# Kernel optimization log

Hardware: AMD Instinct MI355X
Metric: run time of the kernel (lower is better)

Reference implementation:

```python
import jax, jax.numpy as jnp
import numpy as np

B, S = 4096, 128
POS_RANK, DIR_RANK = 10, 4
WIDTH = 256
POS_DIM = POS_RANK * 6  # 60
DIR_DIM = DIR_RANK * 6  # 24
SKIPS = (4,)


def _pe(x, rank):
    # x: [N, 3] -> [N, 6*rank]; sin/cos of x scaled by 2^i for i in 0..rank-1
    freqs = (2.0 ** jnp.arange(rank)).astype(x.dtype)        # [L]
    xf = x[..., None] * freqs                                 # [N, 3, L]
    enc = jnp.concatenate([jnp.sin(xf), jnp.cos(xf)], axis=-1)  # [N, 3, 2L]
    return enc.reshape(x.shape[0], -1)


def _linear_init(key, fan_in, fan_out):
    k1, k2 = jax.random.split(key)
    bound = 1.0 / np.sqrt(fan_in)
    W = jax.random.uniform(k1, (fan_in, fan_out), jnp.float32, -bound, bound)
    b = jax.random.uniform(k2, (fan_out,), jnp.float32, -bound, bound)
    return W, b


def setup_inputs() -> dict:
    key = jax.random.key(0)
    ks = jax.random.split(key, 16)
    inp = {
        "input_pos": jax.random.normal(ks[0], (B, S, 3), jnp.float32),
        "input_dir": jax.random.normal(ks[1], (B, S, 3), jnp.float32),
    }
    # trunk layers: in-dims follow skip-concat structure
    in_dims = [POS_DIM] + [WIDTH + POS_DIM if (i in SKIPS) else WIDTH for i in range(7)]
    for i, d_in in enumerate(in_dims):
        W, b = _linear_init(ks[2 + i], d_in, WIDTH)
        inp[f"W{i}"] = W
        inp[f"b{i}"] = b
    inp["Wd"], inp["bd"] = _linear_init(ks[10], WIDTH, 1)
    inp["Wc0"], inp["bc0"] = _linear_init(ks[11], WIDTH + DIR_DIM, WIDTH // 2)
    inp["Wc1"], inp["bc1"] = _linear_init(ks[12], WIDTH // 2, 3)
    return inp


def reference(input_pos, input_dir,
              W0, b0, W1, b1, W2, b2, W3, b3, W4, b4, W5, b5, W6, b6, W7, b7,
              Wd, bd, Wc0, bc0, Wc1, bc1):
    Ws = [W0, W1, W2, W3, W4, W5, W6, W7]
    bs = [b0, b1, b2, b3, b4, b5, b6, b7]
    b, s, _ = input_pos.shape
    embed_pos = _pe(input_pos.reshape(-1, 3), POS_RANK)  # [N, 60]
    embed_dir = _pe(input_dir.reshape(-1, 3), DIR_RANK)  # [N, 24]
    hx = embed_pos
    for i, (W, bb) in enumerate(zip(Ws, bs)):
        hx = jax.nn.relu(hx @ W + bb)
        if i in SKIPS:
            hx = jnp.concatenate([hx, embed_pos], axis=1)
    density = (hx @ Wd + bd).reshape(b, s)
    dir_feat = jnp.concatenate([hx, embed_dir], axis=1)  # [N, 280]
    color = (jax.nn.relu(dir_feat @ Wc0 + bc0) @ Wc1 + bc1).reshape(b, s, 3)
    return density, color
```

## Files before the change

kernel.cpp:

```cpp
#include <hip/hip_runtime.h>
#include <hip/hip_bf16.h>

using bf16 = __bf16;
typedef __bf16 bf16x8 __attribute__((ext_vector_type(8)));
typedef __bf16 bf16x4 __attribute__((ext_vector_type(4)));
typedef float  f32x4  __attribute__((ext_vector_type(4)));

#define MFMA16(a, b, c) __builtin_amdgcn_mfma_f32_16x16x32_bf16((a), (b), (c), 0, 0, 0)

constexpr int P0  = 0;
constexpr int P1  = 16384;
constexpr int P2  = 81920;
constexpr int P3  = 147456;
constexpr int P4  = 212992;
constexpr int P5  = 278528;
constexpr int P6  = 360448;
constexpr int P7  = 425984;
constexpr int PD  = 491520;
constexpr int PC0 = 495616;
constexpr int PC1 = 532480;

constexpr int NPTS = 4096 * 128;
constexpr int MT = 128;
constexpr int PTILES = MT / 16;
constexpr int NCHUNK = 40;
constexpr int CH = MT * 8;


struct PackArgs {
    const float* src[11];
    int K[11], N[11], Ntiles[11], tasks[11], dstoff[11];
};

__global__ void nerf_pack(PackArgs pa, bf16* __restrict__ dst) {
    int idx = blockIdx.x * 256 + threadIdx.x;
    for (int l = 0; l < 11; ++l) {
        if (idx < pa.tasks[l]) {
            const int lane = idx & 63;
            const int blk  = idx >> 6;
            const int nt   = blk % pa.Ntiles[l];
            const int kt   = blk / pa.Ntiles[l];
            const int kb   = kt * 32 + (lane >> 4) * 8;
            const int n    = nt * 16 + (lane & 15);
            const float* s = pa.src[l];
            const int K = pa.K[l], N = pa.N[l];
            bf16x8 v;
#pragma unroll
            for (int j = 0; j < 8; ++j) {
                int k = kb + j;
                v[j] = (bf16)((k < K && n < N) ? s[(size_t)k * N + n] : 0.f);
            }
            *(bf16x8*)(dst + pa.dstoff[l] + (size_t)idx * 8) = v;
            return;
        }
        idx -= pa.tasks[l];
    }
}

template <int KP, int N, bool RELU, int MODE, bool HAZARD, int COFF>
__device__ __forceinline__ void layer(bf16* H,
                                      const bf16* __restrict__ wp,
                                      const float* __restrict__ bias,
                                      float* __restrict__ gout, int m0) {
    constexpr int NW     = 8;
    constexpr int NTILES = N / 16;
    constexpr int NT_W   = (NTILES >= 8) ? 4 : 1;
    constexpr int CG     = NTILES / NT_W;
    static_assert(CG <= NW && NW % CG == 0, "wave split");
    constexpr int NPG0   = NW / CG;
    constexpr int NPG    = (NPG0 > PTILES) ? PTILES : NPG0;
    constexpr int PT_W   = PTILES / NPG;
    static_assert(NPG == NPG0 || (MODE != 0 && !HAZARD),
                  "idle waves only allowed in barrier-free modes");
    constexpr int KT = KP / 32;
    constexpr int C0 = COFF >> 3;

    const int tid  = threadIdx.x;
    const int lane = tid & 63;
    const int w    = tid >> 6;

    if constexpr (NPG != NPG0) {
        if (w / CG >= NPG) return;
    }

    const int l15  = lane & 15;
    const int quad = lane >> 4;
    const int nt0  = (w % CG) * NT_W;
    const int pt0  = (w / CG) * PT_W;

    const bf16* ar = H + (C0 + quad) * CH + (pt0 * 16 + l15) * 8;

    f32x4 acc[PT_W][NT_W];
    if constexpr (MODE == 0) {
#pragma unroll
        for (int nt = 0; nt < NT_W; ++nt) {
            f32x4 b4 = *(const f32x4*)(bias + (nt0 + nt) * 16 + quad * 4);
#pragma unroll
            for (int pt = 0; pt < PT_W; ++pt) acc[pt][nt] = b4;
        }
    } else if constexpr (MODE == 1) {
        const float bv = bias[0];
        f32x4 t = {bv, bv, bv, bv};
#pragma unroll
        for (int pt = 0; pt < PT_W; ++pt) acc[pt][0] = t;
    } else {
        f32x4 t = {bias[0], bias[1], bias[2], 0.f};
#pragma unroll
        for (int pt = 0; pt < PT_W; ++pt) acc[pt][0] = t;
    }

#pragma unroll 2
    for (int kt = 0; kt < KT; ++kt) {
        bf16x8 wf[NT_W];
#pragma unroll
        for (int nt = 0; nt < NT_W; ++nt)
            wf[nt] = *(const bf16x8*)(wp + ((size_t)(kt * NTILES + nt0 + nt) * 64 + lane) * 8);
#pragma unroll
        for (int pt = 0; pt < PT_W; ++pt) {
            bf16x8 af = *(const bf16x8*)(ar + kt * (4 * CH) + pt * 128);
#pragma unroll
            for (int nt = 0; nt < NT_W; ++nt)
                acc[pt][nt] = MFMA16(wf[nt], af, acc[pt][nt]);
        }
    }
    if (HAZARD) __syncthreads();

    if constexpr (MODE == 0) {
        bf16* wr = H + (nt0 * 2 + (quad >> 1)) * CH + (pt0 * 16 + l15) * 8 + (quad & 1) * 4;
#pragma unroll
        for (int pt = 0; pt < PT_W; ++pt) {
#pragma unroll
            for (int nt = 0; nt < NT_W; ++nt) {
                f32x4 a = acc[pt][nt];
                bf16x4 o;
#pragma unroll
                for (int r = 0; r < 4; ++r) {
                    float v = a[r];
                    if (RELU) v = v > 0.f ? v : 0.f;
                    o[r] = (bf16)v;
                }
                *(bf16x4*)(wr + nt * (2 * CH) + pt * 128) = o;
            }
        }
        __syncthreads();
    } else if constexpr (MODE == 1) {
        if (quad == 0) {
#pragma unroll
            for (int pt = 0; pt < PT_W; ++pt)
                gout[m0 + (pt0 + pt) * 16 + l15] = acc[pt][0][0];
        }
    } else {
        if (quad == 0) {
#pragma unroll
            for (int pt = 0; pt < PT_W; ++pt) {
                const size_t p3 = (size_t)(m0 + (pt0 + pt) * 16 + l15) * 3;
                gout[p3 + 0] = acc[pt][0][0];
                gout[p3 + 1] = acc[pt][0][1];
                gout[p3 + 2] = acc[pt][0][2];
            }
        }
    }
}

__global__ __launch_bounds__(512, 4)
void nerf_main(const float* __restrict__ pos, const float* __restrict__ dir,
               const float* __restrict__ b0, const float* __restrict__ b1,
               const float* __restrict__ b2, const float* __restrict__ b3,
               const float* __restrict__ b4, const float* __restrict__ b5,
               const float* __restrict__ b6, const float* __restrict__ b7,
               const float* __restrict__ bd, const float* __restrict__ bc0,
               const float* __restrict__ bc1,
               const bf16* __restrict__ wpk, float* __restrict__ out) {
    __shared__ __align__(16) bf16 H[NCHUNK * CH];

    const int m0 = blockIdx.x * MT;
    const int tid = threadIdx.x;

    {
        const int row = tid >> 2;
        const int sub = tid & 3;
        const size_t pb = (size_t)(m0 + row) * 3;
        float xs[3] = { pos[pb], pos[pb + 1], pos[pb + 2] };
#pragma unroll
        for (int h = 0; h < 2; ++h) {
            bf16x8 v;
#pragma unroll
            for (int j = 0; j < 8; ++j) {
                const int col = sub * 16 + h * 8 + j;
                float t = 0.f;
                if (col < 60) {
                    const int c = col / 20, rem = col % 20, s = rem / 10, i = rem % 10;
                    const float arg = xs[c] * (float)(1 << i);
                    t = s ? __cosf(arg) : __sinf(arg);
                }
                v[j] = (bf16)t;
            }
            *(bf16x8*)(H + (32 + sub * 2 + h) * CH + row * 8) = v;
        }
    }
    __syncthreads();

    layer<64,  256, true, 0, false, 256>(H, wpk + P0, b0, nullptr, m0);
    layer<256, 256, true, 0, true,  0  >(H, wpk + P1, b1, nullptr, m0);
    layer<256, 256, true, 0, true,  0  >(H, wpk + P2, b2, nullptr, m0);
    layer<256, 256, true, 0, true,  0  >(H, wpk + P3, b3, nullptr, m0);
    layer<256, 256, true, 0, true,  0  >(H, wpk + P4, b4, nullptr, m0);
    layer<320, 256, true, 0, true,  0  >(H, wpk + P5, b5, nullptr, m0);
    layer<256, 256, true, 0, true,  0  >(H, wpk + P6, b6, nullptr, m0);
    layer<256, 256, true, 0, true,  0  >(H, wpk + P7, b7, nullptr, m0);

    layer<256, 16, false, 1, false, 0>(H, wpk + PD, bd, out, m0);

    {
        const int row = tid >> 2;
        const int sub = tid & 3;
        const size_t db = (size_t)(m0 + row) * 3;
        float ds[3] = { dir[db], dir[db + 1], dir[db + 2] };
        bf16x8 v;
#pragma unroll
        for (int j = 0; j < 8; ++j) {
            const int col = sub * 8 + j;
            float t = 0.f;
            if (col < 24) {
                const int c = col / 8, rem = col % 8, s = rem / 4, i = rem % 4;
                const float arg = ds[c] * (float)(1 << i);
                t = s ? __cosf(arg) : __sinf(arg);
            }
            v[j] = (bf16)t;
        }
        *(bf16x8*)(H + (32 + sub) * CH + row * 8) = v;
    }
    __syncthreads();

    layer<288, 128, true, 0, true,  0>(H, wpk + PC0, bc0, nullptr, m0);
    layer<128, 16, false, 2, false, 0>(H, wpk + PC1, bc1, out + NPTS, m0);
}

__global__ void nerf_sentinel(float* __restrict__ out, float val) {
    if (threadIdx.x == 0 && blockIdx.x == 0) out[0] = val;
}

extern "C" void kernel_launch(void* const* d_in, const int* in_sizes, int n_in,
                              void* d_out, int out_size, void* d_ws, size_t ws_size,
                              hipStream_t stream) {
    static const int exp2[24] = {
        1572864, 1572864,
        15360, 256, 65536, 256, 65536, 256, 65536, 256,
        65536, 256, 80896, 256, 65536, 256, 65536, 256,
        256, 1, 35840, 128, 384, 3
    };
    int bad = -1;
    if (n_in != 24) bad = 99;
    else {
        for (int i = 0; i < 24; ++i)
            if (in_sizes[i] != exp2[i]) { bad = i; break; }
    }
    if (bad < 0 && out_size != NPTS * 4) bad = 97;
    if (bad >= 0) {
        nerf_sentinel<<<1, 64, 0, stream>>>((float*)d_out, 20000.f + 100.f * bad);
        return;
    }

    static const int wi[11] = {2, 4, 6, 8, 10, 12, 14, 16, 18, 20, 22};
    static const int Ks[11] = {60, 256, 256, 256, 256, 316, 256, 256, 256, 280, 128};
    static const int Ns[11] = {256, 256, 256, 256, 256, 256, 256, 256, 1, 128, 3};
    static const int Kp[11] = {64, 256, 256, 256, 256, 320, 256, 256, 256, 288, 128};
    static const int Np[11] = {256, 256, 256, 256, 256, 256, 256, 256, 16, 128, 16};

    PackArgs pa;
    int off = 0, total_tasks = 0;
    for (int l = 0; l < 11; ++l) {
        pa.src[l]    = (const float*)d_in[wi[l]];
        pa.K[l]      = Ks[l];
        pa.N[l]      = Ns[l];
        pa.Ntiles[l] = Np[l] / 16;
        pa.tasks[l]  = (Kp[l] / 32) * (Np[l] / 16) * 64;
        pa.dstoff[l] = off;
        off += pa.tasks[l] * 8;
        total_tasks += pa.tasks[l];
    }
    bf16* wpk = (bf16*)d_ws;

    nerf_pack<<<(total_tasks + 255) / 256, 256, 0, stream>>>(pa, wpk);

    nerf_main<<<NPTS / MT, 512, 0, stream>>>(
        (const float*)d_in[0], (const float*)d_in[1],
        (const float*)d_in[3], (const float*)d_in[5], (const float*)d_in[7],
        (const float*)d_in[9], (const float*)d_in[11], (const float*)d_in[13],
        (const float*)d_in[15], (const float*)d_in[17], (const float*)d_in[19],
        (const float*)d_in[21], (const float*)d_in[23],
        wpk, (float*)d_out);
}
```

Baseline: 571.9 us.

## Switch MLP layers from 16x16x32 to 32x32x16 bf16 MFMA tiles

Replaces the 16x16x32 MFMA with the 32x32x16 variant throughout the fused NeRF MLP. Weight packing, LDS activation addressing, bias initialisation and output writeback are all reworked for 32-wide tiles, and the small density and color heads are padded to N=32. The larger tile issues fewer MFMA and LDS fragment loads per FLOP and should raise matrix-core throughput. It also adds s_setprio around the MFMA block. In exchange it needs more accumulator registers per wave and wastes more compute on the padded output heads.

```diff
diff --git a/kernel.cpp b/kernel.cpp
--- a/kernel.cpp
+++ b/kernel.cpp
@@ -5,8 +5,9 @@
 typedef __bf16 bf16x8 __attribute__((ext_vector_type(8)));
 typedef __bf16 bf16x4 __attribute__((ext_vector_type(4)));
 typedef float  f32x4  __attribute__((ext_vector_type(4)));
-
-#define MFMA16(a, b, c) __builtin_amdgcn_mfma_f32_16x16x32_bf16((a), (b), (c), 0, 0, 0)
+typedef float  f32x16 __attribute__((ext_vector_type(16)));
+
+#define MFMA32(a, b, c) __builtin_amdgcn_mfma_f32_32x32x16_bf16((a), (b), (c), 0, 0, 0)
 
 constexpr int P0  = 0;
 constexpr int P1  = 16384;
@@ -17,12 +18,11 @@
 constexpr int P6  = 360448;
 constexpr int P7  = 425984;
 constexpr int PD  = 491520;
-constexpr int PC0 = 495616;
-constexpr int PC1 = 532480;
+constexpr int PC0 = 499712;
+constexpr int PC1 = 536576;
 
 constexpr int NPTS = 4096 * 128;
 constexpr int MT = 128;
-constexpr int PTILES = MT / 16;
 constexpr int NCHUNK = 40;
 constexpr int CH = MT * 8;
 
@@ -40,8 +40,8 @@
             const int blk  = idx >> 6;
             const int nt   = blk % pa.Ntiles[l];
             const int kt   = blk / pa.Ntiles[l];
-            const int kb   = kt * 32 + (lane >> 4) * 8;
-            const int n    = nt * 16 + (lane & 15);
+            const int kb   = kt * 16 + (lane >> 5) * 8;
+            const int n    = nt * 32 + (lane & 31);
             const float* s = pa.src[l];
             const int K = pa.K[l], N = pa.N[l];
             bf16x8 v;
@@ -62,17 +62,17 @@
                                       const bf16* __restrict__ wp,
                                       const float* __restrict__ bias,
                                       float* __restrict__ gout, int m0) {
-    constexpr int NW     = 8;
-    constexpr int NTILES = N / 16;
-    constexpr int NT_W   = (NTILES >= 8) ? 4 : 1;
-    constexpr int CG     = NTILES / NT_W;
+    constexpr int NW   = 8;
+    constexpr int NT32 = N / 32;
+    constexpr int CG   = NT32;
     static_assert(CG <= NW && NW % CG == 0, "wave split");
-    constexpr int NPG0   = NW / CG;
-    constexpr int NPG    = (NPG0 > PTILES) ? PTILES : NPG0;
-    constexpr int PT_W   = PTILES / NPG;
+    constexpr int NPG0 = NW / CG;
+    constexpr int PT32 = MT / 32;
+    constexpr int NPG  = (NPG0 > PT32) ? PT32 : NPG0;
+    constexpr int PT_W = PT32 / NPG;
     static_assert(NPG == NPG0 || (MODE != 0 && !HAZARD),
                   "idle waves only allowed in barrier-free modes");
-    constexpr int KT = KP / 32;
+    constexpr int KT = KP / 16;
     constexpr int C0 = COFF >> 3;
 
     const int tid  = threadIdx.x;
@@ -83,80 +83,86 @@
         if (w / CG >= NPG) return;
     }
 
-    const int l15  = lane & 15;
-    const int quad = lane >> 4;
-    const int nt0  = (w % CG) * NT_W;
-    const int pt0  = (w / CG) * PT_W;
-
-    const bf16* ar = H + (C0 + quad) * CH + (pt0 * 16 + l15) * 8;
-
-    f32x4 acc[PT_W][NT_W];
+    const int l31 = lane & 31;
+    const int h   = lane >> 5;
+    const int nt0 = w % CG;
+    const int pt0 = (w / CG) * PT_W;
+
+    const bf16* ar = H + (C0 + h) * CH + (pt0 * 32 + l31) * 8;
+    const bf16* wr0 = wp + ((size_t)nt0 * 64 + lane) * 8;
+
+    f32x16 acc[PT_W];
     if constexpr (MODE == 0) {
 #pragma unroll
-        for (int nt = 0; nt < NT_W; ++nt) {
-            f32x4 b4 = *(const f32x4*)(bias + (nt0 + nt) * 16 + quad * 4);
-#pragma unroll
-            for (int pt = 0; pt < PT_W; ++pt) acc[pt][nt] = b4;
+        for (int q = 0; q < 4; ++q) {
+            f32x4 bq = *(const f32x4*)(bias + nt0 * 32 + q * 8 + 4 * h);
+#pragma unroll
+            for (int pt = 0; pt < PT_W; ++pt) {
+#pragma unroll
+                for (int i = 0; i < 4; ++i) acc[pt][4 * q + i] = bq[i];
+            }
         }
     } else if constexpr (MODE == 1) {
         const float bv = bias[0];
-        f32x4 t = {bv, bv, bv, bv};
-#pragma unroll
-        for (int pt = 0; pt < PT_W; ++pt) acc[pt][0] = t;
+#pragma unroll
+        for (int pt = 0; pt < PT_W; ++pt) {
+#pragma unroll
+            for (int i = 0; i < 16; ++i) acc[pt][i] = (i == 0) ? bv : 0.f;
+        }
     } else {
-        f32x4 t = {bias[0], bias[1], bias[2], 0.f};
-#pragma unroll
-        for (int pt = 0; pt < PT_W; ++pt) acc[pt][0] = t;
+#pragma unroll
+        for (int pt = 0; pt < PT_W; ++pt) {
+#pragma unroll
+            for (int i = 0; i < 16; ++i) acc[pt][i] = (i < 3) ? bias[i] : 0.f;
+        }
     }
 
 #pragma unroll 2
     for (int kt = 0; kt < KT; ++kt) {
-        bf16x8 wf[NT_W];
-#pragma unroll
-        for (int nt = 0; nt < NT_W; ++nt)
-            wf[nt] = *(const bf16x8*)(wp + ((size_t)(kt * NTILES + nt0 + nt) * 64 + lane) * 8);
+        bf16x8 wf = *(const bf16x8*)(wr0 + (size_t)kt * NT32 * 512);
+        bf16x8 af[PT_W];
+#pragma unroll
+        for (int pt = 0; pt < PT_W; ++pt)
+            af[pt] = *(const bf16x8*)(ar + kt * (2 * CH) + pt * 256);
+        __builtin_amdgcn_s_setprio(1);
+#pragma unroll
+        for (int pt = 0; pt < PT_W; ++pt)
+            acc[pt] = MFMA32(wf, af[pt], acc[pt]);
+        __builtin_amdgcn_s_setprio(0);
+    }
+    if (HAZARD) __syncthreads();
+
+    if constexpr (MODE == 0) {
+        bf16* wrp = H + (nt0 * 4) * CH + (pt0 * 32 + l31) * 8 + 4 * h;
 #pragma unroll
         for (int pt = 0; pt < PT_W; ++pt) {
-            bf16x8 af = *(const bf16x8*)(ar + kt * (4 * CH) + pt * 128);
-#pragma unroll
-            for (int nt = 0; nt < NT_W; ++nt)
-                acc[pt][nt] = MFMA16(wf[nt], af, acc[pt][nt]);
-        }
-    }
-    if (HAZARD) __syncthreads();
-
-    if constexpr (MODE == 0) {
-        bf16* wr = H + (nt0 * 2 + (quad >> 1)) * CH + (pt0 * 16 + l15) * 8 + (quad & 1) * 4;
-#pragma unroll
-        for (int pt = 0; pt < PT_W; ++pt) {
-#pragma unroll
-            for (int nt = 0; nt < NT_W; ++nt) {
-                f32x4 a = acc[pt][nt];
+#pragma unroll
+            for (int q = 0; q < 4; ++q) {
                 bf16x4 o;
 #pragma unroll
-                for (int r = 0; r < 4; ++r) {
-                    float v = a[r];
+                for (int i = 0; i < 4; ++i) {
+                    float v = acc[pt][4 * q + i];
                     if (RELU) v = v > 0.f ? v : 0.f;
-                    o[r] = (bf16)v;
+                    o[i] = (bf16)v;
                 }
-                *(bf16x4*)(wr + nt * (2 * CH) + pt * 128) = o;
+                *(bf16x4*)(wrp + q * CH + pt * 256) = o;
             }
         }
         __syncthreads();
     } else if constexpr (MODE == 1) {
-        if (quad == 0) {
+        if (h == 0) {
 #pragma unroll
             for (int pt = 0; pt < PT_W; ++pt)
-                gout[m0 + (pt0 + pt) * 16 + l15] = acc[pt][0][0];
+                gout[m0 + (pt0 + pt) * 32 + l31] = acc[pt][0];
         }
     } else {
-        if (quad == 0) {
+        if (h == 0) {
 #pragma unroll
             for (int pt = 0; pt < PT_W; ++pt) {
-                const size_t p3 = (size_t)(m0 + (pt0 + pt) * 16 + l15) * 3;
-                gout[p3 + 0] = acc[pt][0][0];
-                gout[p3 + 1] = acc[pt][0][1];
-                gout[p3 + 2] = acc[pt][0][2];
+                const size_t p3 = (size_t)(m0 + (pt0 + pt) * 32 + l31) * 3;
+                gout[p3 + 0] = acc[pt][0];
+                gout[p3 + 1] = acc[pt][1];
+                gout[p3 + 2] = acc[pt][2];
             }
         }
     }
@@ -209,7 +215,7 @@
     layer<256, 256, true, 0, true,  0  >(H, wpk + P6, b6, nullptr, m0);
     layer<256, 256, true, 0, true,  0  >(H, wpk + P7, b7, nullptr, m0);
 
-    layer<256, 16, false, 1, false, 0>(H, wpk + PD, bd, out, m0);
+    layer<256, 32, false, 1, false, 0>(H, wpk + PD, bd, out, m0);
 
     {
         const int row = tid >> 2;
@@ -233,7 +239,7 @@
     __syncthreads();
 
     layer<288, 128, true, 0, true,  0>(H, wpk + PC0, bc0, nullptr, m0);
-    layer<128, 16, false, 2, false, 0>(H, wpk + PC1, bc1, out + NPTS, m0);
+    layer<128, 32, false, 2, false, 0>(H, wpk + PC1, bc1, out + NPTS, m0);
 }
 
 __global__ void nerf_sentinel(float* __restrict__ out, float val) {
@@ -265,7 +271,7 @@
     static const int Ks[11] = {60, 256, 256, 256, 256, 316, 256, 256, 256, 280, 128};
     static const int Ns[11] = {256, 256, 256, 256, 256, 256, 256, 256, 1, 128, 3};
     static const int Kp[11] = {64, 256, 256, 256, 256, 320, 256, 256, 256, 288, 128};
-    static const int Np[11] = {256, 256, 256, 256, 256, 256, 256, 256, 16, 128, 16};
+    static const int Np[11] = {256, 256, 256, 256, 256, 256, 256, 256, 32, 128, 32};
 
     PackArgs pa;
     int off = 0, total_tasks = 0;
@@ -273,8 +279,8 @@
         pa.src[l]    = (const float*)d_in[wi[l]];
         pa.K[l]      = Ks[l];
         pa.N[l]      = Ns[l];
-        pa.Ntiles[l] = Np[l] / 16;
-        pa.tasks[l]  = (Kp[l] / 32) * (Np[l] / 16) * 64;
+        pa.Ntiles[l] = Np[l] / 32;
+        pa.tasks[l]  = (Kp[l] / 16) * (Np[l] / 32) * 64;
         pa.dstoff[l] = off;
         off += pa.tasks[l] * 8;
         total_tasks += pa.tasks[l];
```

New measurement: 658.6 us. 1.15x slower.
